# Kernel tuning notes

Measured on AMD Instinct MI355X. Metric: run time of the kernel, lower is better.

## Reference

```python
import jax, jax.numpy as jnp
import numpy as np

D_MODEL = 1024
N_HEADS = 16
HEAD_DIM = 64


def setup_inputs() -> dict:
    key = jax.random.key(0)
    ks = jax.random.split(key, 9)
    B, T, C = 4, 2048, D_MODEL
    s = 1.0 / np.sqrt(C)
    return {
        "x": jax.random.normal(ks[0], (B, T, C), jnp.float32),
        "wq": jax.random.normal(ks[1], (C, C), jnp.float32) * s,
        "bq": jnp.zeros((C,), jnp.float32),
        "wk": jax.random.normal(ks[2], (C, C), jnp.float32) * s,
        "bk": jnp.zeros((C,), jnp.float32),
        "wv": jax.random.normal(ks[3], (C, C), jnp.float32) * s,
        "bv": jnp.zeros((C,), jnp.float32),
        "wo": jax.random.normal(ks[4], (C, C), jnp.float32) * s,
        "bo": jnp.zeros((C,), jnp.float32),
    }


def reference(x, wq, bq, wk, bk, wv, bv, wo, bo):
    B, T, C = x.shape
    H, Dh = N_HEADS, HEAD_DIM
    # projections -> (B, H, T, Dh)
    def split_heads(t):
        return t.reshape(B, T, H, Dh).transpose(0, 2, 1, 3)
    q = split_heads(x @ wq + bq)
    k = split_heads(x @ wk + bk)
    v = split_heads(x @ wv + bv)
    scale = 1.0 / jnp.sqrt(jnp.asarray(Dh, x.dtype))
    scores = jnp.einsum("bhqd,bhkd->bhqk", q, k) * scale  # (B,H,T,T)
    causal = jnp.tril(jnp.ones((T, T), bool))
    scores = jnp.where(causal, scores, jnp.asarray(-jnp.inf, x.dtype))
    attn = jax.nn.softmax(scores, axis=-1)
    out = jnp.einsum("bhqk,bhkd->bhqd", attn, v)
    out = out.transpose(0, 2, 1, 3).reshape(B, T, C)
    return out @ wo + bo
```

## Files before the change

kernel.cpp:

```cpp
#include <hip/hip_runtime.h>
#include <hip/hip_bf16.h>
#include <stdint.h>

#define D_MODEL 1024
#define NHEADS 16
#define HDIM 64
#define BATCH 4
#define SEQ 2048
#define M_ROWS (BATCH*SEQ)
#define BHTD ((size_t)BATCH*NHEADS*SEQ*HDIM)

typedef __attribute__((ext_vector_type(8))) short bf16x8;
typedef __attribute__((ext_vector_type(4))) float f32x4;
typedef __attribute__((ext_vector_type(16))) float f32x16;
typedef __attribute__((address_space(1))) uint32_t as1_u32;
typedef __attribute__((address_space(3))) uint32_t as3_u32;

__device__ __forceinline__ void gload_lds16(const void* g, void* l) {
    __builtin_amdgcn_global_load_lds((const as1_u32*)(uintptr_t)g,
                                     (as3_u32*)(uintptr_t)l, 16, 0, 0);
}

__device__ __forceinline__ short f2bf(float f) {
    __hip_bfloat16 h = __float2bfloat16(f);
    return *reinterpret_cast<short*>(&h);
}

__device__ __forceinline__ uint32_t cvtpk_bf16(float lo, float hi) {
    uint32_t r;
    asm("v_cvt_pk_bf16_f32 %0, %1, %2" : "=v"(r) : "v"(lo), "v"(hi));
    return r;
}

__device__ __forceinline__ float fexp2(float x) {
    return __builtin_amdgcn_exp2f(x);
}

__global__ __launch_bounds__(256) void prep_k(const float* __restrict__ x,
                                              const float* __restrict__ wq,
                                              const float* __restrict__ wk,
                                              const float* __restrict__ wv,
                                              const float* __restrict__ wo,
                                              short* __restrict__ xb,
                                              short* __restrict__ qkvT,
                                              short* __restrict__ woT) {
    __shared__ float tile[32][33];
    int tid = threadIdx.x;
    int bid = blockIdx.x;
    if (bid < 8192) {
        int i = (bid * 256 + tid) * 4;
        float4 v = *(const float4*)&x[i];
        short4 r;
        r.x = f2bf(v.x); r.y = f2bf(v.y); r.z = f2bf(v.z); r.w = f2bf(v.w);
        *(short4*)&xb[i] = r;
    } else {
        int b2 = bid - 8192;
        int bx = b2 & 31, by = (b2 >> 5) & 31, z = b2 >> 10;
        const float* src = (z == 0) ? wq : (z == 1) ? wk : (z == 2) ? wv : wo;
        short* dst = (z < 3) ? (qkvT + (size_t)z * D_MODEL * D_MODEL) : woT;
        int tx = tid & 31, ty = tid >> 5;
#pragma unroll
        for (int r = 0; r < 32; r += 8)
            tile[ty + r][tx] = src[(size_t)(by * 32 + ty + r) * D_MODEL + bx * 32 + tx];
        __syncthreads();
#pragma unroll
        for (int r = 0; r < 32; r += 8)
            dst[(size_t)(bx * 32 + ty + r) * D_MODEL + by * 32 + tx] = f2bf(tile[tx][ty + r]);
    }
}

template <int MODE>
__global__ __launch_bounds__(256, 2) void gemm128(const short* __restrict__ A,
                                                  const short* __restrict__ Bt,
                                                  const float* __restrict__ b0,
                                                  const float* __restrict__ b1,
                                                  const float* __restrict__ b2,
                                                  short* __restrict__ outb,
                                                  float* __restrict__ outf,
                                                  int K) {
    __shared__ short As[2][128 * 64];
    __shared__ short Bs[2][128 * 64];
    int tid = threadIdx.x;
    int lane = tid & 63, wid = tid >> 6;
    int wr = wid >> 1, wc = wid & 1;
    int lr = lane & 15, lg = lane >> 4;
    int mb = blockIdx.x * 128;
    int nb = blockIdx.y * 128;
    int srow = tid >> 3, kseg = tid & 7;

    f32x4 acc[4][4] = {};
    int nk = K / 64;

    auto STAGE = [&](int bufi, int kb) {
#pragma unroll
        for (int si = 0; si < 4; ++si) {
            int row = srow + si * 32;
            int sp = kseg ^ (row & 7);
            gload_lds16(A + (size_t)(mb + row) * K + kb + sp * 8, &As[bufi][row * 64 + kseg * 8]);
            gload_lds16(Bt + (size_t)(nb + row) * K + kb + sp * 8, &Bs[bufi][row * 64 + kseg * 8]);
        }
    };

    STAGE(0, 0);
    for (int kt = 0; kt < nk; ++kt) {
        int buf = kt & 1;
        if (kt + 1 < nk) {
            STAGE(buf ^ 1, (kt + 1) * 64);
            asm volatile("s_waitcnt vmcnt(8)" ::: "memory");
        } else {
            asm volatile("s_waitcnt vmcnt(0)" ::: "memory");
        }
        __builtin_amdgcn_s_barrier();
        __builtin_amdgcn_sched_barrier(0);
        bf16x8 af[4][2], bfv[4][2];
#pragma unroll
        for (int ms = 0; ms < 4; ++ms) {
            int row = wr * 64 + ms * 16 + lr;
            af[ms][0] = *(const bf16x8*)&As[buf][row * 64 + ((lg ^ (row & 7)) << 3)];
        }
#pragma unroll
        for (int ns = 0; ns < 4; ++ns) {
            int row = wc * 64 + ns * 16 + lr;
            bfv[ns][0] = *(const bf16x8*)&Bs[buf][row * 64 + ((lg ^ (row & 7)) << 3)];
        }
        __builtin_amdgcn_sched_barrier(0);
#pragma unroll
        for (int ms = 0; ms < 4; ++ms) {
            int row = wr * 64 + ms * 16 + lr;
            af[ms][1] = *(const bf16x8*)&As[buf][row * 64 + (((4 + lg) ^ (row & 7)) << 3)];
        }
#pragma unroll
        for (int ns = 0; ns < 4; ++ns) {
            int row = wc * 64 + ns * 16 + lr;
            bfv[ns][1] = *(const bf16x8*)&Bs[buf][row * 64 + (((4 + lg) ^ (row & 7)) << 3)];
        }
        __builtin_amdgcn_sched_barrier(0);
        asm volatile("s_waitcnt lgkmcnt(8)" ::: "memory");
        __builtin_amdgcn_sched_barrier(0);
        __builtin_amdgcn_s_setprio(1);
#pragma unroll
        for (int ms = 0; ms < 4; ++ms)
#pragma unroll
            for (int ns = 0; ns < 4; ++ns)
                acc[ms][ns] = __builtin_amdgcn_mfma_f32_16x16x32_bf16(af[ms][0], bfv[ns][0], acc[ms][ns], 0, 0, 0);
        __builtin_amdgcn_s_setprio(0);
        asm volatile("s_waitcnt lgkmcnt(0)" ::: "memory");
        __builtin_amdgcn_sched_barrier(0);
        __builtin_amdgcn_s_barrier();
        __builtin_amdgcn_sched_barrier(0);
        __builtin_amdgcn_s_setprio(1);
#pragma unroll
        for (int ms = 0; ms < 4; ++ms)
#pragma unroll
            for (int ns = 0; ns < 4; ++ns)
                acc[ms][ns] = __builtin_amdgcn_mfma_f32_16x16x32_bf16(af[ms][1], bfv[ns][1], acc[ms][ns], 0, 0, 0);
        __builtin_amdgcn_s_setprio(0);
    }
#pragma unroll
    for (int ms = 0; ms < 4; ++ms) {
        int row0 = mb + wr * 64 + ms * 16 + lg * 4;
#pragma unroll
        for (int ns = 0; ns < 4; ++ns) {
            int col = nb + wc * 64 + ns * 16 + lr;
            if (MODE == 0) {
                int sec = col >> 10;
                int nn = col & 1023;
                float bias = (sec == 0) ? b0[nn] : (sec == 1) ? b1[nn] : b2[nn];
                int h = nn >> 6, d = nn & 63;
                if (sec == 2) {
                    int bb = row0 >> 11, t0 = row0 & 2047;
                    short4 pk;
#pragma unroll
                    for (int j = 0; j < 4; ++j)
                        *(((short*)&pk) + j) = f2bf(acc[ms][ns][j] + bias);
                    *(short4*)&outb[2 * BHTD + (((size_t)(bb * NHEADS + h)) * HDIM + d) * SEQ + t0] = pk;
                } else {
#pragma unroll
                    for (int j = 0; j < 4; ++j) {
                        int m = row0 + j;
                        int bb = m >> 11, t = m & 2047;
                        float v = acc[ms][ns][j] + bias;
                        if (sec == 0) v *= 0.18033689f;
                        outb[(size_t)sec * BHTD + (((size_t)(bb * NHEADS + h)) * SEQ + t) * HDIM + d] = f2bf(v);
                    }
                }
            } else {
                float bias = b0[col];
#pragma unroll
                for (int j = 0; j < 4; ++j)
                    outf[(size_t)(row0 + j) * D_MODEL + col] = acc[ms][ns][j] + bias;
            }
        }
    }
}

__global__ __launch_bounds__(512, 4) void attn_kernel(const short* __restrict__ Q,
                                                      const short* __restrict__ Kb,
                                                      const short* __restrict__ VTg,
                                                      short* __restrict__ attn_out) {
    __shared__ short Ks[2][4096];
    __shared__ short Vt[2][4096];
    int tid = threadIdx.x, lane = tid & 63, w = tid >> 6;
    int l31 = lane & 31, hi = lane >> 5;

    int linear = blockIdx.x + 8 * blockIdx.y;
    int bh = 8 * (linear & 7) + ((linear >> 3) & 7);
    int qt = 7 - (linear >> 6);
    int b = bh >> 4, h = bh & 15;
    const short* Qp  = Q   + (size_t)bh * SEQ * HDIM;
    const short* Kp  = Kb  + (size_t)bh * SEQ * HDIM;
    const short* VTp = VTg + (size_t)bh * HDIM * SEQ;

    int srow = tid >> 3;
    int kseg = tid & 7;
    int sp   = kseg ^ (srow & 7);
    int swl  = (l31 & 7) << 3;

    int qbase = qt << 8;
    int qrow0 = qbase + w * 32;
    int myq = qrow0 + l31;

    bf16x8 qf[4];
#pragma unroll
    for (int ks = 0; ks < 4; ++ks)
        qf[ks] = *(const bf16x8*)&Qp[(size_t)myq * HDIM + ks * 16 + hi * 8];

    f32x16 o0 = {}, o1 = {};
    float lsum = 0.f;

    int nkb = 4 * qt + 4;
    int buf = 0;
    gload_lds16(Kp + (size_t)srow * HDIM + sp * 8, &Ks[buf][srow * 64 + kseg * 8]);
    gload_lds16(VTp + (size_t)srow * SEQ + sp * 8, &Vt[buf][srow * 64 + kseg * 8]);
    for (int kvb = 0; kvb < nkb; ++kvb) {
        int tb = kvb << 6;
        __syncthreads();
        if (kvb + 1 < nkb) {
            int tb2 = tb + 64, bn = buf ^ 1;
            gload_lds16(Kp + (size_t)(tb2 + srow) * HDIM + sp * 8, &Ks[bn][srow * 64 + kseg * 8]);
            gload_lds16(VTp + (size_t)srow * SEQ + tb2 + sp * 8, &Vt[bn][srow * 64 + kseg * 8]);
        }
        int dq = qrow0 - tb;
        if (dq >= 0) {
            bool has1 = dq >= 32;
            const short* ksb = &Ks[buf][0];
            const short* vtb = &Vt[buf][0];
            f32x16 s0 = {}, s1 = {};
            __builtin_amdgcn_s_setprio(1);
#pragma unroll
            for (int ks = 0; ks < 4; ++ks) {
                bf16x8 kf = *(const bf16x8*)&ksb[l31 * 64 + ((ks * 16 + hi * 8) ^ swl)];
                s0 = __builtin_amdgcn_mfma_f32_32x32x16_bf16(kf, qf[ks], s0, 0, 0, 0);
            }
            if (has1) {
#pragma unroll
                for (int ks = 0; ks < 4; ++ks) {
                    bf16x8 kf = *(const bf16x8*)&ksb[(32 + l31) * 64 + ((ks * 16 + hi * 8) ^ swl)];
                    s1 = __builtin_amdgcn_mfma_f32_32x32x16_bf16(kf, qf[ks], s1, 0, 0, 0);
                }
            }
            __builtin_amdgcn_s_setprio(0);
            if (dq == 0) {
                int thr = l31 - 4 * hi;
#pragma unroll
                for (int r = 0; r < 16; ++r) {
                    int crow = (r & 3) + 8 * (r >> 2);
                    s0[r] = (crow > thr) ? -3e38f : s0[r];
                }
            } else if (dq == 32) {
                int thr = l31 - 4 * hi;
#pragma unroll
                for (int r = 0; r < 16; ++r) {
                    int crow = (r & 3) + 8 * (r >> 2);
                    s1[r] = (crow > thr) ? -3e38f : s1[r];
                }
            }
#pragma unroll
            for (int r = 0; r < 16; ++r) s0[r] = fexp2(s0[r]);
            if (has1) {
#pragma unroll
                for (int r = 0; r < 16; ++r) s1[r] = fexp2(s1[r]);
            }
            float pa0, pa1, pa2, pa3;
            pa0 = s0[0] + s0[4]; pa1 = s0[1] + s0[5];
            pa2 = s0[2] + s0[6]; pa3 = s0[3] + s0[7];
            pa0 += s0[8] + s0[12]; pa1 += s0[9] + s0[13];
            pa2 += s0[10] + s0[14]; pa3 += s0[11] + s0[15];
            if (has1) {
                pa0 += s1[0] + s1[4]; pa1 += s1[1] + s1[5];
                pa2 += s1[2] + s1[6]; pa3 += s1[3] + s1[7];
                pa0 += s1[8] + s1[12]; pa1 += s1[9] + s1[13];
                pa2 += s1[10] + s1[14]; pa3 += s1[11] + s1[15];
            }
            float ps = (pa0 + pa1) + (pa2 + pa3);
            ps += __shfl_xor(ps, 32);
            lsum += ps;
            uint32_t W0[8], W1[8];
#pragma unroll
            for (int u = 0; u < 8; ++u) W0[u] = cvtpk_bf16(s0[2 * u], s0[2 * u + 1]);
            if (has1) {
#pragma unroll
                for (int u = 0; u < 8; ++u) W1[u] = cvtpk_bf16(s1[2 * u], s1[2 * u + 1]);
            }
            uint32_t g0[4], g1[4];
#pragma unroll
            for (int ab = 0; ab < 4; ++ab) {
                int ap = ab >> 1, bb = ab & 1;
                uint32_t swv = hi ? W0[4 * ap + bb] : W0[4 * ap + 2 + bb];
                g0[ab] = __shfl_xor(swv, 32);
            }
            if (has1) {
#pragma unroll
                for (int ab = 0; ab < 4; ++ab) {
                    int ap = ab >> 1, bb = ab & 1;
                    uint32_t swv = hi ? W1[4 * ap + bb] : W1[4 * ap + 2 + bb];
                    g1[ab] = __shfl_xor(swv, 32);
                }
            }
            union { uint32_t u[4]; bf16x8 v; } pa[4];
#pragma unroll
            for (int ks = 0; ks < 4; ++ks) {
                const uint32_t* W = (ks < 2) ? W0 : W1;
                const uint32_t* g = (ks < 2) ? g0 : g1;
                int ap = ks & 1;
                pa[ks].u[0] = hi ? g[ap * 2 + 0] : W[4 * ap + 0];
                pa[ks].u[1] = hi ? g[ap * 2 + 1] : W[4 * ap + 1];
                pa[ks].u[2] = hi ? W[4 * ap + 2] : g[ap * 2 + 0];
                pa[ks].u[3] = hi ? W[4 * ap + 3] : g[ap * 2 + 1];
            }
            __builtin_amdgcn_s_setprio(1);
#pragma unroll
            for (int ks = 0; ks < 4; ++ks) {
                if (ks < 2 || has1) {
                    bf16x8 vf0 = *(const bf16x8*)&vtb[l31 * 64 + ((ks * 16 + hi * 8) ^ swl)];
                    o0 = __builtin_amdgcn_mfma_f32_32x32x16_bf16(vf0, pa[ks].v, o0, 0, 0, 0);
                    bf16x8 vf1 = *(const bf16x8*)&vtb[(32 + l31) * 64 + ((ks * 16 + hi * 8) ^ swl)];
                    o1 = __builtin_amdgcn_mfma_f32_32x32x16_bf16(vf1, pa[ks].v, o1, 0, 0, 0);
                }
            }
            __builtin_amdgcn_s_setprio(0);
        }
        buf ^= 1;
    }
    float inv = 1.0f / lsum;
    short* outp = &attn_out[((size_t)(b * SEQ) + myq) * D_MODEL + h * HDIM + 4 * hi];
#pragma unroll
    for (int rq = 0; rq < 4; ++rq) {
        uint32_t a0 = cvtpk_bf16(o0[4 * rq + 0] * inv, o0[4 * rq + 1] * inv);
        uint32_t a1 = cvtpk_bf16(o0[4 * rq + 2] * inv, o0[4 * rq + 3] * inv);
        uint2 pk0 = {a0, a1};
        *(uint2*)(outp + 8 * rq) = pk0;
        uint32_t b0_ = cvtpk_bf16(o1[4 * rq + 0] * inv, o1[4 * rq + 1] * inv);
        uint32_t b1_ = cvtpk_bf16(o1[4 * rq + 2] * inv, o1[4 * rq + 3] * inv);
        uint2 pk1 = {b0_, b1_};
        *(uint2*)(outp + 32 + 8 * rq) = pk1;
    }
}

extern "C" void kernel_launch(void* const* d_in, const int* in_sizes, int n_in,
                              void* d_out, int out_size, void* d_ws, size_t ws_size,
                              hipStream_t stream) {
    const float* x  = (const float*)d_in[0];
    const float* wq = (const float*)d_in[1];
    const float* bq = (const float*)d_in[2];
    const float* wk = (const float*)d_in[3];
    const float* bk = (const float*)d_in[4];
    const float* wv = (const float*)d_in[5];
    const float* bv = (const float*)d_in[6];
    const float* wo = (const float*)d_in[7];
    const float* bo = (const float*)d_in[8];
    float* out = (float*)d_out;

    char* ws = (char*)d_ws;
    size_t off = 0;
    auto alloc = [&](size_t bytes) {
        void* p = ws + off;
        off += (bytes + 255) & ~(size_t)255;
        return p;
    };
    short* xb   = (short*)alloc((size_t)M_ROWS * D_MODEL * 2);
    short* qkvT = (short*)alloc((size_t)3 * D_MODEL * D_MODEL * 2);
    short* woT  = (short*)alloc((size_t)D_MODEL * D_MODEL * 2);
    short* qkv  = (short*)alloc((size_t)3 * BHTD * 2);
    short* ao   = (short*)alloc((size_t)M_ROWS * D_MODEL * 2);

    prep_k<<<dim3(8192 + 4096), dim3(256), 0, stream>>>(
        x, wq, wk, wv, wo, xb, qkvT, woT);
    gemm128<0><<<dim3(M_ROWS / 128, 3 * D_MODEL / 128), dim3(256), 0, stream>>>(
        xb, qkvT, bq, bk, bv, qkv, nullptr, D_MODEL);
    attn_kernel<<<dim3(8, 64), dim3(512), 0, stream>>>(
        qkv, qkv + BHTD, qkv + 2 * BHTD, ao);
    gemm128<1><<<dim3(M_ROWS / 128, D_MODEL / 128), dim3(256), 0, stream>>>(
        ao, woT, bo, nullptr, nullptr, nullptr, out, D_MODEL);
}
```

Baseline: 150.8 us.

## Software-pipeline PV MFMA behind next QK^T and shrink attention blocks to 128 queries

The attention kernel now uses 256-thread blocks that each cover 128 query rows, doubling the grid, so causal work is spread more evenly and more blocks can be resident. The P·V product for one KV tile is deferred to the next iteration, so it interleaves with the next tile's QK^T and softmax. This needs a triple-buffered V tile and P fragments carried across iterations in registers. The aim is to hide exp/shuffle latency behind MFMA, at the cost of more register pressure and extra K/V reloads per query.

```diff
diff --git a/kernel.cpp b/kernel.cpp
--- a/kernel.cpp
+++ b/kernel.cpp
@@ -194,18 +194,18 @@
     }
 }
 
-__global__ __launch_bounds__(512, 4) void attn_kernel(const short* __restrict__ Q,
+__global__ __launch_bounds__(256, 4) void attn_kernel(const short* __restrict__ Q,
                                                       const short* __restrict__ Kb,
                                                       const short* __restrict__ VTg,
                                                       short* __restrict__ attn_out) {
     __shared__ short Ks[2][4096];
-    __shared__ short Vt[2][4096];
+    __shared__ short Vt[3][4096];
     int tid = threadIdx.x, lane = tid & 63, w = tid >> 6;
     int l31 = lane & 31, hi = lane >> 5;
 
     int linear = blockIdx.x + 8 * blockIdx.y;
     int bh = 8 * (linear & 7) + ((linear >> 3) & 7);
-    int qt = 7 - (linear >> 6);
+    int qt = 15 - (linear >> 6);
     int b = bh >> 4, h = bh & 15;
     const short* Qp  = Q   + (size_t)bh * SEQ * HDIM;
     const short* Kp  = Kb  + (size_t)bh * SEQ * HDIM;
@@ -216,7 +216,7 @@
     int sp   = kseg ^ (srow & 7);
     int swl  = (l31 & 7) << 3;
 
-    int qbase = qt << 8;
+    int qbase = qt << 7;
     int qrow0 = qbase + w * 32;
     int myq = qrow0 + l31;
 
@@ -228,24 +228,31 @@
     f32x16 o0 = {}, o1 = {};
     float lsum = 0.f;
 
-    int nkb = 4 * qt + 4;
-    int buf = 0;
-    gload_lds16(Kp + (size_t)srow * HDIM + sp * 8, &Ks[buf][srow * 64 + kseg * 8]);
-    gload_lds16(VTp + (size_t)srow * SEQ + sp * 8, &Vt[buf][srow * 64 + kseg * 8]);
+    auto STG = [&](int kb, int vb, int tb) {
+#pragma unroll
+        for (int si = 0; si < 2; ++si) {
+            int row = srow + si * 32;
+            gload_lds16(Kp + (size_t)(tb + row) * HDIM + sp * 8, &Ks[kb][row * 64 + kseg * 8]);
+            gload_lds16(VTp + (size_t)row * SEQ + tb + sp * 8, &Vt[vb][row * 64 + kseg * 8]);
+        }
+    };
+
+    int nkb = 2 * qt + 2;
+    STG(0, 0, 0);
+    bool prevAct = false, prevHas1 = false;
+    int prevVb = 0;
+    union PA { uint32_t u[4]; bf16x8 v; };
+    PA pav[4];
     for (int kvb = 0; kvb < nkb; ++kvb) {
         int tb = kvb << 6;
         __syncthreads();
-        if (kvb + 1 < nkb) {
-            int tb2 = tb + 64, bn = buf ^ 1;
-            gload_lds16(Kp + (size_t)(tb2 + srow) * HDIM + sp * 8, &Ks[bn][srow * 64 + kseg * 8]);
-            gload_lds16(VTp + (size_t)srow * SEQ + tb2 + sp * 8, &Vt[bn][srow * 64 + kseg * 8]);
-        }
+        if (kvb + 1 < nkb)
+            STG((kvb + 1) & 1, (kvb + 1) % 3, tb + 64);
         int dq = qrow0 - tb;
-        if (dq >= 0) {
-            bool has1 = dq >= 32;
-            const short* ksb = &Ks[buf][0];
-            const short* vtb = &Vt[buf][0];
-            f32x16 s0 = {}, s1 = {};
+        bool act = dq >= 0, has1 = dq >= 32;
+        const short* ksb = &Ks[kvb & 1][0];
+        f32x16 s0 = {}, s1 = {};
+        if (act) {
             __builtin_amdgcn_s_setprio(1);
 #pragma unroll
             for (int ks = 0; ks < 4; ++ks) {
@@ -260,6 +267,22 @@
                 }
             }
             __builtin_amdgcn_s_setprio(0);
+        }
+        if (prevAct) {
+            const short* vtb = &Vt[prevVb][0];
+            __builtin_amdgcn_s_setprio(1);
+#pragma unroll
+            for (int ks = 0; ks < 4; ++ks) {
+                if (ks < 2 || prevHas1) {
+                    bf16x8 vf0 = *(const bf16x8*)&vtb[l31 * 64 + ((ks * 16 + hi * 8) ^ swl)];
+                    o0 = __builtin_amdgcn_mfma_f32_32x32x16_bf16(vf0, pav[ks].v, o0, 0, 0, 0);
+                    bf16x8 vf1 = *(const bf16x8*)&vtb[(32 + l31) * 64 + ((ks * 16 + hi * 8) ^ swl)];
+                    o1 = __builtin_amdgcn_mfma_f32_32x32x16_bf16(vf1, pav[ks].v, o1, 0, 0, 0);
+                }
+            }
+            __builtin_amdgcn_s_setprio(0);
+        }
+        if (act) {
             if (dq == 0) {
                 int thr = l31 - 4 * hi;
 #pragma unroll
@@ -317,30 +340,36 @@
                     g1[ab] = __shfl_xor(swv, 32);
                 }
             }
-            union { uint32_t u[4]; bf16x8 v; } pa[4];
-#pragma unroll
-            for (int ks = 0; ks < 4; ++ks) {
-                const uint32_t* W = (ks < 2) ? W0 : W1;
-                const uint32_t* g = (ks < 2) ? g0 : g1;
-                int ap = ks & 1;
-                pa[ks].u[0] = hi ? g[ap * 2 + 0] : W[4 * ap + 0];
-                pa[ks].u[1] = hi ? g[ap * 2 + 1] : W[4 * ap + 1];
-                pa[ks].u[2] = hi ? W[4 * ap + 2] : g[ap * 2 + 0];
-                pa[ks].u[3] = hi ? W[4 * ap + 3] : g[ap * 2 + 1];
-            }
-            __builtin_amdgcn_s_setprio(1);
-#pragma unroll
-            for (int ks = 0; ks < 4; ++ks) {
-                if (ks < 2 || has1) {
-                    bf16x8 vf0 = *(const bf16x8*)&vtb[l31 * 64 + ((ks * 16 + hi * 8) ^ swl)];
-                    o0 = __builtin_amdgcn_mfma_f32_32x32x16_bf16(vf0, pa[ks].v, o0, 0, 0, 0);
-                    bf16x8 vf1 = *(const bf16x8*)&vtb[(32 + l31) * 64 + ((ks * 16 + hi * 8) ^ swl)];
-                    o1 = __builtin_amdgcn_mfma_f32_32x32x16_bf16(vf1, pa[ks].v, o1, 0, 0, 0);
-                }
-            }
-            __builtin_amdgcn_s_setprio(0);
-        }
-        buf ^= 1;
+#pragma unroll
+            for (int ks = 0; ks < 2; ++ks) {
+                pav[ks].u[0] = hi ? g0[ks * 2 + 0] : W0[4 * ks + 0];
+                pav[ks].u[1] = hi ? g0[ks * 2 + 1] : W0[4 * ks + 1];
+                pav[ks].u[2] = hi ? W0[4 * ks + 2] : g0[ks * 2 + 0];
+                pav[ks].u[3] = hi ? W0[4 * ks + 3] : g0[ks * 2 + 1];
+            }
+            if (has1) {
+#pragma unroll
+                for (int ks = 0; ks < 2; ++ks) {
+                    pav[2 + ks].u[0] = hi ? g1[ks * 2 + 0] : W1[4 * ks + 0];
+                    pav[2 + ks].u[1] = hi ? g1[ks * 2 + 1] : W1[4 * ks + 1];
+                    pav[2 + ks].u[2] = hi ? W1[4 * ks + 2] : g1[ks * 2 + 0];
+                    pav[2 + ks].u[3] = hi ? W1[4 * ks + 3] : g1[ks * 2 + 1];
+                }
+            }
+        }
+        prevAct = act; prevHas1 = has1; prevVb = kvb % 3;
+    }
+    if (prevAct) {
+        const short* vtb = &Vt[prevVb][0];
+#pragma unroll
+        for (int ks = 0; ks < 4; ++ks) {
+            if (ks < 2 || prevHas1) {
+                bf16x8 vf0 = *(const bf16x8*)&vtb[l31 * 64 + ((ks * 16 + hi * 8) ^ swl)];
+                o0 = __builtin_amdgcn_mfma_f32_32x32x16_bf16(vf0, pav[ks].v, o0, 0, 0, 0);
+                bf16x8 vf1 = *(const bf16x8*)&vtb[(32 + l31) * 64 + ((ks * 16 + hi * 8) ^ swl)];
+                o1 = __builtin_amdgcn_mfma_f32_32x32x16_bf16(vf1, pav[ks].v, o1, 0, 0, 0);
+            }
+        }
     }
     float inv = 1.0f / lsum;
     short* outp = &attn_out[((size_t)(b * SEQ) + myq) * D_MODEL + h * HDIM + 4 * hi];
@@ -388,7 +417,7 @@
         x, wq, wk, wv, wo, xb, qkvT, woT);
     gemm128<0><<<dim3(M_ROWS / 128, 3 * D_MODEL / 128), dim3(256), 0, stream>>>(
         xb, qkvT, bq, bk, bv, qkv, nullptr, D_MODEL);
-    attn_kernel<<<dim3(8, 64), dim3(512), 0, stream>>>(
+    attn_kernel<<<dim3(8, 128), dim3(256), 0, stream>>>(
         qkv, qkv + BHTD, qkv + 2 * BHTD, ao);
     gemm128<1><<<dim3(M_ROWS / 128, D_MODEL / 128), dim3(256), 0, stream>>>(
         ao, woT, bo, nullptr, nullptr, nullptr, out, D_MODEL);
```

Result: slower. 196.6 us (+30.4%).
